# Kernel tuning notes

Hardware: AMD Instinct MI355X
Metric: run time of the kernel (lower is better)

## Reference

```python
import jax, jax.numpy as jnp
from jax import lax
import numpy as np

B, L, C_CH, HH, WW = 2, 5, 64, 100, 352
DOWNSAMPLE_RATE = 2
DISCRETE_RATIO = 0.4  # voxel_size[0]
KEEP_FRAC = 4  # keep top H*W//4 locations per non-ego agent


def setup_inputs() -> dict:
    key = jax.random.key(0)
    k1, k2, k3, k4 = jax.random.split(key, 4)
    N = B * L
    x = jax.random.normal(k1, (N, C_CH, HH, WW), jnp.float32)
    psm = jax.random.normal(k2, (N, 2, HH, WW), jnp.float32)
    record_len = jnp.full((B,), L, dtype=jnp.int32)
    # homogeneous transforms: identity + small perturbation so warps stay mostly in-bounds
    eye = jnp.eye(4, dtype=jnp.float32)
    pairwise_t_matrix = eye + 0.05 * jax.random.normal(k3, (B, L, L, 4, 4), jnp.float32)
    fuse_w = 0.02 * jax.random.normal(k4, (C_CH, C_CH, 7, 7), jnp.float32)
    fuse_b = jnp.zeros((C_CH,), jnp.float32)
    return {"x": x, "psm": psm, "record_len": record_len,
            "pairwise_t_matrix": pairwise_t_matrix, "fuse_w": fuse_w, "fuse_b": fuse_b}


def _bilinear_sample(img, px, py):
    # img [C,H,W]; px,py pixel coords [H,W]; zero padding (grid_sample padding_mode='zeros')
    C, H, W = img.shape
    x0 = jnp.floor(px); y0 = jnp.floor(py)
    wx1 = px - x0; wx0 = 1.0 - wx1
    wy1 = py - y0; wy0 = 1.0 - wy1

    def gather(yy, xx):
        yi = jnp.clip(yy, 0, H - 1).astype(jnp.int32)
        xi = jnp.clip(xx, 0, W - 1).astype(jnp.int32)
        val = img[:, yi, xi]  # [C,H,W]
        valid = ((yy >= 0) & (yy <= H - 1) & (xx >= 0) & (xx <= W - 1)).astype(img.dtype)
        return val * valid

    return (gather(y0, x0) * (wy0 * wx0) + gather(y0, x0 + 1) * (wy0 * wx1)
            + gather(y0 + 1, x0) * (wy1 * wx0) + gather(y0 + 1, x0 + 1) * (wy1 * wx1))


def _affine_warp(img, theta):
    # warp_affine_simple: F.affine_grid + F.grid_sample, align_corners=False
    C, H, W = img.shape
    ys = (jnp.arange(H, dtype=img.dtype) + 0.5) * (2.0 / H) - 1.0
    xs = (jnp.arange(W, dtype=img.dtype) + 0.5) * (2.0 / W) - 1.0
    gy, gx = jnp.meshgrid(ys, xs, indexing='ij')  # [H,W]
    src_x = theta[0, 0] * gx + theta[0, 1] * gy + theta[0, 2]
    src_y = theta[1, 0] * gx + theta[1, 1] * gy + theta[1, 2]
    px = (src_x + 1.0) * (W * 0.5) - 0.5
    py = (src_y + 1.0) * (H * 0.5) - 0.5
    return _bilinear_sample(img, px, py)


def _forward(x, psm, pairwise_t_matrix, fuse_w, fuse_b):
    N, C, H, W = x.shape
    Bp, Lp = pairwise_t_matrix.shape[:2]
    # take 2x3 affine part: rows [0,1], cols [0,1,3]
    t = pairwise_t_matrix[..., :2, :][..., jnp.array([0, 1, 3])]  # [B,L,L,2,3]
    scale = jnp.array([[1.0, H / W, 2.0 / (DOWNSAMPLE_RATE * DISCRETE_RATIO * W)],
                       [W / H, 1.0, 2.0 / (DOWNSAMPLE_RATE * DISCRETE_RATIO * H)]], dtype=x.dtype)
    t = t * scale
    # ego row (t_matrix[0, :N]): warp every agent into the ego frame
    thetas = t[:, 0].reshape(N, 2, 3)  # [N,2,3]

    # Communication: confidence map = sigmoid(max over anchor channels)
    conf = jax.nn.sigmoid(jnp.max(psm, axis=1, keepdims=True))  # [N,1,H,W]

    warp = jax.vmap(_affine_warp)
    x_w = warp(x, thetas)          # [N,C,H,W]
    conf_w = warp(conf, thetas)    # [N,1,H,W]

    # confidence-driven sparsification: keep top H*W//KEEP_FRAC locations per agent
    K = (H * W) // KEEP_FRAC
    flat = conf_w.reshape(N, H * W)
    kth = lax.top_k(flat, K)[0][:, -1]                      # [N]
    mask = (flat >= kth[:, None]).astype(x.dtype).reshape(N, 1, H, W)
    is_ego = (jnp.arange(N) % Lp) == 0                      # ego keeps everything
    mask = jnp.where(is_ego[:, None, None, None], jnp.ones_like(mask), mask)

    sparse = x_w * mask
    fused = lax.conv_general_dilated(sparse, fuse_w, (1, 1), [(3, 3), (3, 3)],
                                     dimension_numbers=('NCHW', 'OIHW', 'NCHW'))
    fused = fused + fuse_b[None, :, None, None]
    # per-scene fusion across agents (mean aggregation)
    out = fused.reshape(Bp, Lp, C, H, W).mean(axis=1)  # [B,C,H,W]
    return out


def reference(x, psm, record_len, pairwise_t_matrix, fuse_w, fuse_b):
    del record_len  # regular case: every scene has L agents
    return _forward(x, psm, pairwise_t_matrix, fuse_w, fuse_b)
```

## Files before the change

kernel.cpp:

```cpp
#include <hip/hip_runtime.h>
#include <hip/hip_bf16.h>

#define HH 100
#define WW 352
#define NB 2
#define LL 5
#define NN 10
#define CCH 64
#define HW (HH*WW)
#define KTOP (HW/4)
#define HP (HH+6)
#define WP 390

typedef __bf16 bf16x8 __attribute__((ext_vector_type(8)));
typedef float f32x4 __attribute__((ext_vector_type(4)));

#define WS_CONF  0u
#define WS_TAU   1408000u
#define WS_WTP   1408064u
#define WS_PAD   1809472u
#define WS_XT    12392512u
#define WS_GH    57448512u
#define PAD_BYTES ((size_t)NB*HP*WP*CCH*2)


__device__ __forceinline__ void load_theta(const float* __restrict__ ptm, int b, int l, float th[6]) {
#pragma clang fp contract(off)
  const float* tb = ptm + ((b*LL + 0)*LL + l)*16;
  th[0] = tb[0] * 1.0f;
  th[1] = tb[1] * (float)(100.0/352.0);
  th[2] = tb[3] * (float)(2.0/(2.0*0.4*352.0));
  th[3] = tb[4] * (float)(352.0/100.0);
  th[4] = tb[5] * 1.0f;
  th[5] = tb[7] * (float)(2.0/(2.0*0.4*100.0));
}

__global__ __launch_bounds__(256) void conf_topk1_kernel(const float* __restrict__ psm,
                                                         const float* __restrict__ ptm,
                                                         float* __restrict__ conf_w,
                                                         unsigned int* __restrict__ gh) {
#pragma clang fp contract(off)
  __shared__ unsigned int hist[16384];
  int s = blockIdx.x;
  int n = blockIdx.y;
  int tid = threadIdx.x;
  for (int i = tid; i < 16384; i += 256) hist[i] = 0u;
  int b = n / LL, l = n % LL;
  float th[6];
  load_theta(ptm, b, l, th);
  const float* p0 = psm + (size_t)(n*2 + 0)*HW;
  const float* p1 = psm + (size_t)(n*2 + 1)*HW;
  __syncthreads();
  int i0 = s * (HW/8);
  for (int i = i0 + tid; i < i0 + HW/8; i += 256) {
    int h = i / WW, w = i - h*WW;
    float gy = ((float)h + 0.5f) * (float)(2.0/100.0) - 1.0f;
    float gx = ((float)w + 0.5f) * (float)(2.0/352.0) - 1.0f;
    float sx = th[0]*gx + th[1]*gy + th[2];
    float sy = th[3]*gx + th[4]*gy + th[5];
    float px = (sx + 1.0f) * ((float)WW * 0.5f) - 0.5f;
    float py = (sy + 1.0f) * ((float)HH * 0.5f) - 0.5f;
    float x0 = floorf(px), y0 = floorf(py);
    float wx1 = px - x0, wx0 = 1.0f - wx1;
    float wy1 = py - y0, wy0 = 1.0f - wy1;
    float yy[2] = {y0, y0 + 1.0f};
    float xx[2] = {x0, x0 + 1.0f};
    float wgt[2][2] = {{wy0*wx0, wy0*wx1}, {wy1*wx0, wy1*wx1}};
    float out = 0.0f;
    for (int iy = 0; iy < 2; ++iy) {
      for (int ix = 0; ix < 2; ++ix) {
        float yv = yy[iy], xv = xx[ix];
        float yc = fminf(fmaxf(yv, 0.0f), (float)(HH-1));
        float xc = fminf(fmaxf(xv, 0.0f), (float)(WW-1));
        int yi = (int)yc, xi = (int)xc;
        int idx = yi*WW + xi;
        float m = fmaxf(p0[idx], p1[idx]);
        float v = 1.0f / (1.0f + expf(-m));
        bool valid = (yv >= 0.0f) && (yv <= (float)(HH-1)) && (xv >= 0.0f) && (xv <= (float)(WW-1));
        out += (valid ? v : 0.0f) * wgt[iy][ix];
      }
    }
    conf_w[(size_t)n*HW + i] = out;
    unsigned int u = __float_as_uint(out);
    atomicAdd(&hist[(u >> 18) & 16383u], 1u);
  }
  __syncthreads();
  for (int i = tid; i < 16384; i += 256) {
    unsigned int c = hist[i];
    if (c) atomicAdd(&gh[n*16384 + i], c);
  }
}

__device__ __forceinline__ unsigned int scan_incl(unsigned int v, int lane, int wid,
                                                  volatile unsigned int* wsum) {
  unsigned int inc = v;
  for (int off = 1; off < 64; off <<= 1) {
    unsigned int o = __shfl_up(inc, off);
    if (lane >= off) inc += o;
  }
  if (lane == 63) wsum[wid] = inc;
  __syncthreads();
  unsigned int wadd = 0;
  for (int w2 = 0; w2 < wid; ++w2) wadd += wsum[w2];
  return inc + wadd;
}

__global__ __launch_bounds__(256) void topk_kernel(const float* __restrict__ conf_w,
                                                   const unsigned int* __restrict__ gh,
                                                   float* __restrict__ tau) {
  __shared__ unsigned int hist[16384];
  __shared__ unsigned int wsum[4];
  __shared__ unsigned int s_pref, s_mask, s_k;
  int n = blockIdx.x;
  int tid = threadIdx.x, lane = tid & 63, wid = tid >> 6;
  const float4* src = (const float4*)(conf_w + (size_t)n*HW);
  if (tid == 0) { s_pref = 0u; s_mask = 0u; s_k = KTOP; }
  __syncthreads();
  const int shifts[3] = {18, 4, 0};
  const int widths[3] = {14, 14, 4};
  for (int r = 0; r < 3; ++r) {
    int shift = shifts[r];
    int nbins = 1 << widths[r];
    unsigned int fmask = (unsigned int)(nbins - 1);
    if (r == 0) {
      for (int i = tid; i < 16384; i += 256) hist[i] = gh[n*16384 + i];
      __syncthreads();
    } else {
      for (int i = tid; i < nbins; i += 256) hist[i] = 0u;
      __syncthreads();
      unsigned int maskhi = s_mask, pref = s_pref;
      for (int i = tid; i < HW/4; i += 256) {
        float4 v = src[i];
        unsigned int u0 = __float_as_uint(v.x);
        unsigned int u1 = __float_as_uint(v.y);
        unsigned int u2 = __float_as_uint(v.z);
        unsigned int u3 = __float_as_uint(v.w);
        if ((u0 & maskhi) == pref) atomicAdd(&hist[(u0 >> shift) & fmask], 1u);
        if ((u1 & maskhi) == pref) atomicAdd(&hist[(u1 >> shift) & fmask], 1u);
        if ((u2 & maskhi) == pref) atomicAdd(&hist[(u2 >> shift) & fmask], 1u);
        if ((u3 & maskhi) == pref) atomicAdd(&hist[(u3 >> shift) & fmask], 1u);
      }
      __syncthreads();
    }
    unsigned int k = s_k;
    int C = nbins >> 8; if (C == 0) C = 1;
    int active = (C * 256 > nbins) ? nbins : 256;
    int top = nbins - 1 - tid*C;
    unsigned int csum = 0u;
    if (tid < active)
      for (int i = 0; i < C; ++i) csum += hist[top - i];
    unsigned int incl = scan_incl(csum, lane, wid, wsum);
    unsigned int excl = incl - csum;
    if (tid < active && excl < k && incl >= k) {
      unsigned int run = excl;
      for (int i = 0; i < C; ++i) {
        unsigned int c = hist[top - i];
        if (run + c >= k) {
          unsigned int bin = (unsigned int)(top - i);
          s_pref = s_pref | (bin << shift);
          s_mask = s_mask | (fmask << shift);
          s_k = k - run;
          break;
        }
        run += c;
      }
    }
    __syncthreads();
  }
  if (tid == 0) tau[n] = __uint_as_float(s_pref);
}

__global__ void pack_w_kernel(const float* __restrict__ fw, __bf16* __restrict__ wtp) {
  int idx = blockIdx.x*256 + threadIdx.x;
  if (idx >= CCH*CCH*49) return;
  int c = idx & 63;
  int k = (idx >> 6) & 63;
  int dydx = idx >> 12;
  wtp[((size_t)dydx*CCH + k)*CCH + c] = (__bf16)fw[((size_t)k*CCH + c)*49 + dydx];
}

__global__ __launch_bounds__(256) void repack_x_kernel(const float* __restrict__ x,
                                                       __bf16* __restrict__ xT) {
  __shared__ float tile[64][65];
  int n = blockIdx.y;
  int px0 = blockIdx.x * 64;
  int tid = threadIdx.x;
  int pxl = tid & 63;
  int c0 = tid >> 6;
  const float* xs = x + (size_t)n*CCH*HW + px0 + pxl;
#pragma unroll
  for (int i = 0; i < 16; ++i) {
    int c = c0 + i*4;
    tile[c][pxl] = xs[(size_t)c*HW];
  }
  __syncthreads();
  int px2 = tid >> 2;
  int cc0 = (tid & 3) * 16;
  __bf16 vv[16];
#pragma unroll
  for (int j = 0; j < 16; ++j) vv[j] = (__bf16)tile[cc0 + j][px2];
  __bf16* dst = xT + ((size_t)n*HW + px0 + px2)*CCH + cc0;
  *reinterpret_cast<bf16x8*>(dst)     = *reinterpret_cast<bf16x8*>(&vv[0]);
  *reinterpret_cast<bf16x8*>(dst + 8) = *reinterpret_cast<bf16x8*>(&vv[8]);
}

__global__ __launch_bounds__(256) void warp_avg_kernel(
    const __bf16* __restrict__ xT, const float* __restrict__ ptm,
    const float* __restrict__ conf_w, const float* __restrict__ tau,
    __bf16* __restrict__ pad) {
  __shared__ float sth[NN][6];
  __shared__ float stau[NN];
  int tid = threadIdx.x;
  if (tid < NN*6) {
    int bl = tid / 6, j = tid - bl*6;
    int bb = bl / LL, ll = bl - bb*LL;
    const float* tb = ptm + ((bb*LL + 0)*LL + ll)*16;
    float v;
    if      (j == 0) v = tb[0] * 1.0f;
    else if (j == 1) v = tb[1] * (float)(100.0/352.0);
    else if (j == 2) v = tb[3] * (float)(2.0/(2.0*0.4*352.0));
    else if (j == 3) v = tb[4] * (float)(352.0/100.0);
    else if (j == 4) v = tb[5] * 1.0f;
    else             v = tb[7] * (float)(2.0/(2.0*0.4*100.0));
    sth[bl][j] = v;
  }
  if (tid >= 64 && tid < 64 + NN) stau[tid - 64] = tau[tid - 64];
  __syncthreads();

  int idx = blockIdx.x*256 + tid;
  int px = idx >> 2;
  int ch0 = (idx & 3) * 16;
  int b = (px >= HW) ? 1 : 0;
  int rem = px - b*HW;
  int h = rem / WW;
  int w = rem - h*WW;
  float acc[16];
#pragma unroll
  for (int i = 0; i < 16; ++i) acc[i] = 0.0f;
  float gy = ((float)h + 0.5f) * (float)(2.0/100.0) - 1.0f;
  float gx = ((float)w + 0.5f) * (float)(2.0/352.0) - 1.0f;
  for (int l = 0; l < LL; ++l) {
    int n = b*LL + l;
    if (l != 0 && !(conf_w[(size_t)n*HW + rem] >= stau[n])) continue;
    float sx = sth[n][0]*gx + sth[n][1]*gy + sth[n][2];
    float sy = sth[n][3]*gx + sth[n][4]*gy + sth[n][5];
    float fpx = (sx + 1.0f) * ((float)WW*0.5f) - 0.5f;
    float fpy = (sy + 1.0f) * ((float)HH*0.5f) - 0.5f;
    float x0 = floorf(fpx), y0 = floorf(fpy);
    float wx1 = fpx - x0, wx0 = 1.0f - wx1;
    float wy1 = fpy - y0, wy0 = 1.0f - wy1;
    float y1 = y0 + 1.0f, x1 = x0 + 1.0f;
    bool vy0 = (y0 >= 0.0f) && (y0 <= (float)(HH-1));
    bool vy1 = (y1 >= 0.0f) && (y1 <= (float)(HH-1));
    bool vx0 = (x0 >= 0.0f) && (x0 <= (float)(WW-1));
    bool vx1 = (x1 >= 0.0f) && (x1 <= (float)(WW-1));
    int yi0 = (int)fminf(fmaxf(y0, 0.0f), (float)(HH-1));
    int yi1 = (int)fminf(fmaxf(y1, 0.0f), (float)(HH-1));
    int xi0 = (int)fminf(fmaxf(x0, 0.0f), (float)(WW-1));
    int xi1 = (int)fminf(fmaxf(x1, 0.0f), (float)(WW-1));
    float wgt[4] = { wy0*wx0 * ((vy0 && vx0) ? 1.0f : 0.0f),
                     wy0*wx1 * ((vy0 && vx1) ? 1.0f : 0.0f),
                     wy1*wx0 * ((vy1 && vx0) ? 1.0f : 0.0f),
                     wy1*wx1 * ((vy1 && vx1) ? 1.0f : 0.0f) };
    int off[4] = { yi0*WW + xi0, yi0*WW + xi1, yi1*WW + xi0, yi1*WW + xi1 };
#pragma unroll
    for (int t4 = 0; t4 < 4; ++t4) {
      if (wgt[t4] == 0.0f) continue;
      float wt = wgt[t4];
      const __bf16* src = xT + ((size_t)n*HW + off[t4])*CCH + ch0;
#pragma unroll
      for (int ch = 0; ch < 2; ++ch) {
        bf16x8 v = *reinterpret_cast<const bf16x8*>(src + ch*8);
#pragma unroll
        for (int e = 0; e < 8; ++e) acc[ch*8 + e] += wt * (float)v[e];
      }
    }
  }
  char* rowb = (char*)pad + (size_t)((b*HP + (h+3))*WP)*128;
  int px_p = w + 3;
  int key = (px_p & 7) << 4;
#pragma unroll
  for (int ch = 0; ch < 2; ++ch) {
    bf16x8 o;
#pragma unroll
    for (int e = 0; e < 8; ++e) o[e] = (__bf16)(acc[ch*8 + e]*0.2f);
    int slotb = (ch0*2 + ch*16) ^ key;
    *reinterpret_cast<bf16x8*>(rowb + (size_t)px_p*128 + slotb) = o;
  }
}


#define AFREAD(DX) do { \
  _Pragma("unroll") for (int m = 0; m < 2; ++m) { \
    af[m][0] = *(const bf16x8*)&wlds[((DX)*32 + m*16 + l16)*64 + cj0*8]; \
    af[m][1] = *(const bf16x8*)&wlds[((DX)*32 + m*16 + l16)*64 + cj1*8]; } } while(0)

__global__ __launch_bounds__(256, 2) void conv_kernel(
    const __bf16* __restrict__ pad, const __bf16* __restrict__ wtp,
    const float* __restrict__ fb, float* __restrict__ out) {
  __shared__ __bf16 wlds[7*32*64];
  __shared__ __bf16 plds[4][4608];
  int tid = threadIdx.x;
  int wave = tid >> 6, lane = tid & 63;
  int quad = lane >> 4, l16 = lane & 15;
  int r8 = lane >> 3, jc = lane & 7;
  int jcr = (jc - r8) & 7;
  int cj0 = (quad + l16) & 7;
  int cj1 = (quad + 4 + l16) & 7;
  int bz = blockIdx.z;
  int b = bz >> 1, kh = bz & 1;
  int h0 = blockIdx.y*4;
  int h = h0 + wave;
  int w0 = blockIdx.x*64;

  f32x4 acc[2][4];
#pragma unroll
  for (int m = 0; m < 2; ++m)
#pragma unroll
    for (int n = 0; n < 4; ++n) acc[m][n] = (f32x4){0.f,0.f,0.f,0.f};

  bf16x8 af[2][2];

#pragma unroll 1
  for (int dy = 0; dy < 7; ++dy) {
    __syncthreads();
    const __bf16* wdy = wtp + dy*28672;
#pragma unroll
    for (int j = 0; j < 7; ++j) {
      int q = wave*7 + j;
      int srcrow = (q >> 2)*64 + kh*32 + (q & 3)*8 + r8;
      __builtin_amdgcn_global_load_lds(
          (const __attribute__((address_space(1))) void*)(wdy + srcrow*64 + jcr*8),
          (__attribute__((address_space(3))) void*)&wlds[q*512], 16, 0, 0);
    }
    const __bf16* prow_g = pad + (size_t)((b*HP + h + dy)*WP + w0)*CCH;
#pragma unroll
    for (int j = 0; j < 9; ++j) {
      __builtin_amdgcn_global_load_lds(
          (const __attribute__((address_space(1))) void*)(prow_g + j*512 + lane*8),
          (__attribute__((address_space(3))) void*)&plds[wave][j*512], 16, 0, 0);
    }
    __syncthreads();
#pragma unroll
    for (int dx = 0; dx < 7; ++dx) {
      AFREAD(dx);
      bf16x8 bf[4][2];
#pragma unroll
      for (int n = 0; n < 4; ++n) {
        int p = dx + n*16 + l16;
        int key = (p & 7) << 4;
#pragma unroll
        for (int kc = 0; kc < 2; ++kc) {
          int slotb = ((quad + 4*kc) << 4) ^ key;
          bf[n][kc] = *(const bf16x8*)((const char*)&plds[wave][0] + p*128 + slotb);
        }
      }
#pragma unroll
      for (int kc = 0; kc < 2; ++kc)
#pragma unroll
        for (int m = 0; m < 2; ++m)
#pragma unroll
          for (int n = 0; n < 4; ++n)
            acc[m][n] = __builtin_amdgcn_mfma_f32_16x16x32_bf16(af[m][kc], bf[n][kc], acc[m][n], 0, 0, 0);
    }
  }

#pragma unroll
  for (int n = 0; n < 4; ++n) {
    int wpix = w0 + n*16 + l16;
    if (wpix < WW) {
#pragma unroll
      for (int m = 0; m < 2; ++m) {
#pragma unroll
        for (int rr = 0; rr < 4; ++rr) {
          int kg = kh*32 + m*16 + quad*4 + rr;
          out[((size_t)(b*CCH + kg)*HH + h)*WW + wpix] = acc[m][n][rr] + fb[kg];
        }
      }
    }
  }
}

extern "C" void kernel_launch(void* const* d_in, const int* in_sizes, int n_in,
                              void* d_out, int out_size, void* d_ws, size_t ws_size,
                              hipStream_t stream) {
  (void)in_sizes; (void)n_in; (void)out_size; (void)ws_size;
  const float* x   = (const float*)d_in[0];
  const float* psm = (const float*)d_in[1];
  const float* ptm = (const float*)d_in[3];
  const float* fw  = (const float*)d_in[4];
  const float* fb  = (const float*)d_in[5];
  float* out = (float*)d_out;
  char* ws = (char*)d_ws;
  float*  conf = (float*)(ws + WS_CONF);
  float*  tau  = (float*)(ws + WS_TAU);
  __bf16* wtp  = (__bf16*)(ws + WS_WTP);
  __bf16* pad  = (__bf16*)(ws + WS_PAD);
  __bf16* xT   = (__bf16*)(ws + WS_XT);
  unsigned int* gh = (unsigned int*)(ws + WS_GH);

  hipMemsetAsync(pad, 0, PAD_BYTES, stream);
  hipMemsetAsync(gh, 0, (size_t)NN*16384*4, stream);
  pack_w_kernel<<<(CCH*CCH*49 + 255)/256, 256, 0, stream>>>(fw, wtp);
  repack_x_kernel<<<dim3(HW/64, NN), 256, 0, stream>>>(x, xT);
  conf_topk1_kernel<<<dim3(8, NN), 256, 0, stream>>>(psm, ptm, conf, gh);
  topk_kernel<<<NN, 256, 0, stream>>>(conf, gh, tau);
  warp_avg_kernel<<<dim3(NB*HW*4/256), 256, 0, stream>>>(xT, ptm, conf, tau, pad);
  conv_kernel<<<dim3(6, 25, NB*2), 256, 0, stream>>>(pad, wtp, fb, out);
}
```

Before: 290.3 us.

## Split confidence warp from histogram, use per-slice histograms stored in output buffer

Separates the confidence warp into its own fully parallel kernel (one thread per pixel, 3000 blocks) and moves the coarse radix histogram into a separate kernel. That kernel writes per-slice partial histograms with plain stores, and topk sums them. This removes the global atomics and the memset of the histogram buffer. The partial histograms are placed in the output buffer as scratch, which conv overwrites later. This adds one extra read pass over conf_w.

```diff
diff --git a/kernel.cpp b/kernel.cpp
--- a/kernel.cpp
+++ b/kernel.cpp
@@ -20,7 +20,6 @@
 #define WS_WTP   1408064u
 #define WS_PAD   1809472u
 #define WS_XT    12392512u
-#define WS_GH    57448512u
 #define PAD_BYTES ((size_t)NB*HP*WP*CCH*2)
 
 
@@ -35,60 +34,66 @@
   th[5] = tb[7] * (float)(2.0/(2.0*0.4*100.0));
 }
 
-__global__ __launch_bounds__(256) void conf_topk1_kernel(const float* __restrict__ psm,
-                                                         const float* __restrict__ ptm,
-                                                         float* __restrict__ conf_w,
-                                                         unsigned int* __restrict__ gh) {
+__global__ void conf_warp_kernel(const float* __restrict__ psm,
+                                 const float* __restrict__ ptm,
+                                 float* __restrict__ conf_w) {
 #pragma clang fp contract(off)
-  __shared__ unsigned int hist[16384];
-  int s = blockIdx.x;
-  int n = blockIdx.y;
-  int tid = threadIdx.x;
-  for (int i = tid; i < 16384; i += 256) hist[i] = 0u;
+  int w = blockIdx.x * 128 + threadIdx.x;
+  int h = blockIdx.y;
+  int n = blockIdx.z;
+  if (w >= WW) return;
   int b = n / LL, l = n % LL;
   float th[6];
   load_theta(ptm, b, l, th);
+  float gy = ((float)h + 0.5f) * (float)(2.0/100.0) - 1.0f;
+  float gx = ((float)w + 0.5f) * (float)(2.0/352.0) - 1.0f;
+  float sx = th[0]*gx + th[1]*gy + th[2];
+  float sy = th[3]*gx + th[4]*gy + th[5];
+  float px = (sx + 1.0f) * ((float)WW * 0.5f) - 0.5f;
+  float py = (sy + 1.0f) * ((float)HH * 0.5f) - 0.5f;
+  float x0 = floorf(px), y0 = floorf(py);
+  float wx1 = px - x0, wx0 = 1.0f - wx1;
+  float wy1 = py - y0, wy0 = 1.0f - wy1;
   const float* p0 = psm + (size_t)(n*2 + 0)*HW;
   const float* p1 = psm + (size_t)(n*2 + 1)*HW;
-  __syncthreads();
-  int i0 = s * (HW/8);
-  for (int i = i0 + tid; i < i0 + HW/8; i += 256) {
-    int h = i / WW, w = i - h*WW;
-    float gy = ((float)h + 0.5f) * (float)(2.0/100.0) - 1.0f;
-    float gx = ((float)w + 0.5f) * (float)(2.0/352.0) - 1.0f;
-    float sx = th[0]*gx + th[1]*gy + th[2];
-    float sy = th[3]*gx + th[4]*gy + th[5];
-    float px = (sx + 1.0f) * ((float)WW * 0.5f) - 0.5f;
-    float py = (sy + 1.0f) * ((float)HH * 0.5f) - 0.5f;
-    float x0 = floorf(px), y0 = floorf(py);
-    float wx1 = px - x0, wx0 = 1.0f - wx1;
-    float wy1 = py - y0, wy0 = 1.0f - wy1;
-    float yy[2] = {y0, y0 + 1.0f};
-    float xx[2] = {x0, x0 + 1.0f};
-    float wgt[2][2] = {{wy0*wx0, wy0*wx1}, {wy1*wx0, wy1*wx1}};
-    float out = 0.0f;
-    for (int iy = 0; iy < 2; ++iy) {
-      for (int ix = 0; ix < 2; ++ix) {
-        float yv = yy[iy], xv = xx[ix];
-        float yc = fminf(fmaxf(yv, 0.0f), (float)(HH-1));
-        float xc = fminf(fmaxf(xv, 0.0f), (float)(WW-1));
-        int yi = (int)yc, xi = (int)xc;
-        int idx = yi*WW + xi;
-        float m = fmaxf(p0[idx], p1[idx]);
-        float v = 1.0f / (1.0f + expf(-m));
-        bool valid = (yv >= 0.0f) && (yv <= (float)(HH-1)) && (xv >= 0.0f) && (xv <= (float)(WW-1));
-        out += (valid ? v : 0.0f) * wgt[iy][ix];
-      }
-    }
-    conf_w[(size_t)n*HW + i] = out;
-    unsigned int u = __float_as_uint(out);
-    atomicAdd(&hist[(u >> 18) & 16383u], 1u);
-  }
-  __syncthreads();
-  for (int i = tid; i < 16384; i += 256) {
-    unsigned int c = hist[i];
-    if (c) atomicAdd(&gh[n*16384 + i], c);
-  }
+  float yy[2] = {y0, y0 + 1.0f};
+  float xx[2] = {x0, x0 + 1.0f};
+  float wgt[2][2] = {{wy0*wx0, wy0*wx1}, {wy1*wx0, wy1*wx1}};
+  float out = 0.0f;
+  for (int iy = 0; iy < 2; ++iy) {
+    for (int ix = 0; ix < 2; ++ix) {
+      float yv = yy[iy], xv = xx[ix];
+      float yc = fminf(fmaxf(yv, 0.0f), (float)(HH-1));
+      float xc = fminf(fmaxf(xv, 0.0f), (float)(WW-1));
+      int yi = (int)yc, xi = (int)xc;
+      int idx = yi*WW + xi;
+      float m = fmaxf(p0[idx], p1[idx]);
+      float v = 1.0f / (1.0f + expf(-m));
+      bool valid = (yv >= 0.0f) && (yv <= (float)(HH-1)) && (xv >= 0.0f) && (xv <= (float)(WW-1));
+      out += (valid ? v : 0.0f) * wgt[iy][ix];
+    }
+  }
+  conf_w[(size_t)n*HW + h*WW + w] = out;
+}
+
+__global__ __launch_bounds__(256) void hist1_kernel(const float* __restrict__ conf_w,
+                                                    unsigned int* __restrict__ gh) {
+  __shared__ unsigned int hist[16384];
+  int s = blockIdx.x, n = blockIdx.y;
+  int tid = threadIdx.x;
+  for (int i = tid; i < 16384; i += 256) hist[i] = 0u;
+  __syncthreads();
+  const float4* src = (const float4*)(conf_w + (size_t)n*HW);
+  for (int f = s*1100 + tid; f < (s+1)*1100; f += 256) {
+    float4 v = src[f];
+    atomicAdd(&hist[(__float_as_uint(v.x) >> 18) & 16383u], 1u);
+    atomicAdd(&hist[(__float_as_uint(v.y) >> 18) & 16383u], 1u);
+    atomicAdd(&hist[(__float_as_uint(v.z) >> 18) & 16383u], 1u);
+    atomicAdd(&hist[(__float_as_uint(v.w) >> 18) & 16383u], 1u);
+  }
+  __syncthreads();
+  unsigned int* dst = gh + ((size_t)s*NN + n)*16384;
+  for (int i = tid; i < 16384; i += 256) dst[i] = hist[i];
 }
 
 __device__ __forceinline__ unsigned int scan_incl(unsigned int v, int lane, int wid,
@@ -123,7 +128,12 @@
     int nbins = 1 << widths[r];
     unsigned int fmask = (unsigned int)(nbins - 1);
     if (r == 0) {
-      for (int i = tid; i < 16384; i += 256) hist[i] = gh[n*16384 + i];
+      for (int i = tid; i < 16384; i += 256) {
+        unsigned int ssum = 0u;
+#pragma unroll
+        for (int s2 = 0; s2 < 8; ++s2) ssum += gh[((size_t)s2*NN + n)*16384 + i];
+        hist[i] = ssum;
+      }
       __syncthreads();
     } else {
       for (int i = tid; i < nbins; i += 256) hist[i] = 0u;
@@ -397,13 +407,13 @@
   __bf16* wtp  = (__bf16*)(ws + WS_WTP);
   __bf16* pad  = (__bf16*)(ws + WS_PAD);
   __bf16* xT   = (__bf16*)(ws + WS_XT);
-  unsigned int* gh = (unsigned int*)(ws + WS_GH);
+  unsigned int* gh = (unsigned int*)d_out;
 
   hipMemsetAsync(pad, 0, PAD_BYTES, stream);
-  hipMemsetAsync(gh, 0, (size_t)NN*16384*4, stream);
+  conf_warp_kernel<<<dim3(3, HH, NN), 128, 0, stream>>>(psm, ptm, conf);
   pack_w_kernel<<<(CCH*CCH*49 + 255)/256, 256, 0, stream>>>(fw, wtp);
   repack_x_kernel<<<dim3(HW/64, NN), 256, 0, stream>>>(x, xT);
-  conf_topk1_kernel<<<dim3(8, NN), 256, 0, stream>>>(psm, ptm, conf, gh);
+  hist1_kernel<<<dim3(8, NN), 256, 0, stream>>>(conf, gh);
   topk_kernel<<<NN, 256, 0, stream>>>(conf, gh, tau);
   warp_avg_kernel<<<dim3(NB*HW*4/256), 256, 0, stream>>>(xT, ptm, conf, tau, pad);
   conv_kernel<<<dim3(6, 25, NB*2), 256, 0, stream>>>(pad, wtp, fb, out);
```

New measurement: 275.1 us. -5.2%, faster.
